# Kernel optimization log

Hardware: AMD Instinct MI355X
Metric: run time of the kernel (lower is better)

The kernel has to match this reference:

```python
import jax, jax.numpy as jnp
import numpy as np

B, P, ENC = 128, 625, 512
A, E, H, V = 256, 256, 512, 70
START_TOK, END_TOK = 68, 69


def setup_inputs() -> dict:
    key = jax.random.key(0)
    ks = jax.random.split(key, 20)
    w = lambda k, shape: jax.random.normal(k, shape, jnp.float32) * 0.02
    return {
        "encoder_out": jax.random.normal(ks[0], (B, P, ENC), jnp.float32),
        "emb": w(ks[1], (V, E)),
        "We": w(ks[2], (ENC, A)), "be": jnp.zeros((A,), jnp.float32),
        "Wd": w(ks[3], (H, A)),   "bd": jnp.zeros((A,), jnp.float32),
        "wf": w(ks[4], (A,)),     "bf": jnp.zeros((), jnp.float32),
        "Wh0": w(ks[5], (ENC, H)), "bh0": jnp.zeros((H,), jnp.float32),
        "Wc0": w(ks[6], (ENC, H)), "bc0": jnp.zeros((H,), jnp.float32),
        "Wb": w(ks[7], (H, ENC)), "bb": jnp.zeros((ENC,), jnp.float32),
        "Wih": w(ks[8], (E + ENC, 4 * H)), "Whh": w(ks[9], (H, 4 * H)),
        "bih": jnp.zeros((4 * H,), jnp.float32), "bhh": jnp.zeros((4 * H,), jnp.float32),
        "Wfc": w(ks[10], (H, V)), "bfc": jnp.zeros((V,), jnp.float32),
        "decode_lengths": 70,
    }


def _decode(encoder_out, emb, We, be, Wd, bd, wf, bf, Wh0, bh0, Wc0, bc0,
            Wb, bb, Wih, Whh, bih, bhh, Wfc, bfc, decode_lengths):
    enc = encoder_out  # [B, P, ENC]
    batch = enc.shape[0]
    # encoder_att projection is constant across timesteps -> hoist out of loop
    att1 = enc @ We + be                      # [B, P, A]
    mean_enc = enc.mean(axis=1)               # [B, ENC]
    h0 = mean_enc @ Wh0 + bh0                 # [B, H]
    c0 = mean_enc @ Wc0 + bc0                 # [B, H]
    emb0 = emb[jnp.full((batch,), START_TOK)]  # [B, E]
    lstm_b = bih + bhh

    def step(carry, _):
        h, c, emb_t, done = carry
        att2 = h @ Wd + bd                                            # [B, A]
        e = jnp.einsum('bpa,a->bp', jax.nn.relu(att1 + att2[:, None, :]), wf) + bf
        alpha = jax.nn.softmax(e, axis=1)                             # [B, P]
        awe = jnp.einsum('bp,bpe->be', alpha, enc)                    # [B, ENC]
        awe = jax.nn.sigmoid(h @ Wb + bb) * awe                       # gated
        gates = jnp.concatenate([emb_t, awe], axis=1) @ Wih + h @ Whh + lstm_b
        i_, f_, g_, o_ = jnp.split(gates, 4, axis=1)                  # torch order i,f,g,o
        c_new = jax.nn.sigmoid(f_) * c + jax.nn.sigmoid(i_) * jnp.tanh(g_)
        h_new = jax.nn.sigmoid(o_) * jnp.tanh(c_new)
        preds = h_new @ Wfc + bfc                                     # [B, V] (dropout eval = id)
        preds_out = jnp.where(done, 0.0, preds)                       # zeros after early break
        done_new = done | (jnp.argmax(preds) == END_TOK)              # flat argmax, as in torch
        emb_new = emb[jnp.argmax(preds, axis=-1)]                     # greedy feedback
        return (h_new, c_new, emb_new, done_new), preds_out

    init = (h0, c0, emb0, jnp.array(False))
    _, preds_seq = jax.lax.scan(step, init, None, length=decode_lengths)
    return jnp.transpose(preds_seq, (1, 0, 2))  # [B, T, V]


def reference(encoder_out, emb, We, be, Wd, bd, wf, bf, Wh0, bh0, Wc0, bc0,
              Wb, bb, Wih, Whh, bih, bhh, Wfc, bfc, decode_lengths):
    return _decode(encoder_out, emb, We, be, Wd, bd, wf, bf, Wh0, bh0, Wc0, bc0,
                   Wb, bb, Wih, Whh, bih, bhh, Wfc, bfc, decode_lengths)
```

## Files before the change

kernel.cpp:

```cpp
#include <hip/hip_runtime.h>
#include <math.h>

#define Bn 128
#define Pn 625
#define ENCn 512
#define An 256
#define En 256
#define Hn 512
#define Vn 70
#define G4n 2048
#define STARTT 68
#define ENDT 69
#define NCHUNK 5
#define PCH 125
#define PSTRIDE 520
#define KSPLIT 16
#define KCH 80


__global__ __launch_bounds__(256) void k_mean(const float* __restrict__ enc,
                                              float* __restrict__ mean_enc) {
  int b = blockIdx.x, t = threadIdx.x;
  const float* e = enc + (size_t)b * Pn * ENCn;
  float s0 = 0.f, s1 = 0.f;
  for (int p = 0; p < Pn; ++p) {
    s0 += e[(size_t)p * ENCn + t];
    s1 += e[(size_t)p * ENCn + t + 256];
  }
  mean_enc[b * ENCn + t] = s0 * (1.0f / 625.0f);
  mean_enc[b * ENCn + t + 256] = s1 * (1.0f / 625.0f);
}

__global__ __launch_bounds__(512) void k_init(const float* __restrict__ mean_enc,
                       const float* __restrict__ Wh0, const float* __restrict__ bh0,
                       const float* __restrict__ Wc0, const float* __restrict__ bc0,
                       const float* __restrict__ emb,
                       float* __restrict__ h0, float* __restrict__ c0,
                       float* __restrict__ emb_t, int* __restrict__ done_arr) {
  int b = blockIdx.x, t = threadIdx.x;
  const float* W = blockIdx.y ? Wc0 : Wh0;
  const float* bias = blockIdx.y ? bc0 : bh0;
  float* out = blockIdx.y ? c0 : h0;
  __shared__ float ms[ENCn];
  ms[t] = mean_enc[b * ENCn + t];
  __syncthreads();
  float s = bias[t];
  for (int k = 0; k < ENCn; ++k) s += ms[k] * W[k * Hn + t];
  out[b * Hn + t] = s;
  if (blockIdx.y == 0 && t < En) emb_t[b * En + t] = emb[STARTT * En + t];
  if (blockIdx.y == 0 && b == 0 && t == 0) done_arr[0] = 0;
}

__global__ __launch_bounds__(256) void k_att1(const float* __restrict__ Am,
                       const float* __restrict__ We,
                       const float* __restrict__ be, float* __restrict__ att1) {
  __shared__ float sA[16][128];
  __shared__ float sB[16][128];
  int n0 = blockIdx.x * 128, m0 = blockIdx.y * 128;
  int t = threadIdx.x;
  int tm = (t >> 4) * 8, tn = (t & 15) * 8;
  float acc[8][8];
#pragma unroll
  for (int i = 0; i < 8; ++i)
#pragma unroll
    for (int j = 0; j < 8; ++j) acc[i][j] = 0.f;
  for (int k0 = 0; k0 < 512; k0 += 16) {
    __syncthreads();
#pragma unroll
    for (int i = 0; i < 8; ++i) {
      int idx = t + i * 256;
      int mm = idx >> 4, kk = idx & 15;
      sA[kk][mm] = Am[(size_t)(m0 + mm) * 512 + k0 + kk];
      int kk2 = idx >> 7, nn = idx & 127;
      sB[kk2][nn] = We[(size_t)(k0 + kk2) * 256 + n0 + nn];
    }
    __syncthreads();
#pragma unroll
    for (int kk = 0; kk < 16; ++kk) {
      float a[8], bq[8];
      *(float4*)&a[0] = *(const float4*)&sA[kk][tm];
      *(float4*)&a[4] = *(const float4*)&sA[kk][tm + 4];
      *(float4*)&bq[0] = *(const float4*)&sB[kk][tn];
      *(float4*)&bq[4] = *(const float4*)&sB[kk][tn + 4];
#pragma unroll
      for (int i = 0; i < 8; ++i)
#pragma unroll
        for (int j = 0; j < 8; ++j) acc[i][j] += a[i] * bq[j];
    }
  }
  float ber[8];
  *(float4*)&ber[0] = *(const float4*)&be[n0 + tn];
  *(float4*)&ber[4] = *(const float4*)&be[n0 + tn + 4];
#pragma unroll
  for (int i = 0; i < 8; ++i) {
    float o[8];
#pragma unroll
    for (int j = 0; j < 8; ++j) o[j] = acc[i][j] + ber[j];
    *(float4*)&att1[(size_t)(m0 + tm + i) * An + n0 + tn] = *(float4*)&o[0];
    *(float4*)&att1[(size_t)(m0 + tm + i) * An + n0 + tn + 4] = *(float4*)&o[4];
  }
}


__global__ __launch_bounds__(256) void k_proj(const float* __restrict__ h,
                       const float* __restrict__ Wd, const float* __restrict__ bd,
                       const float* __restrict__ Wb, const float* __restrict__ bbv,
                       float* __restrict__ att2, float* __restrict__ gate,
                       const float* __restrict__ preds,
                       const int* __restrict__ done_prev, int* __restrict__ done_cur,
                       int do_flat) {
  int t = threadIdx.x;
  if (blockIdx.x == Bn) {
    if (!do_flat) return;
    __shared__ float sv[256];
    __shared__ int si[256];
    float bv = -1e30f; int bi = 0x7fffffff;
    for (int i = t; i < Bn * Vn; i += 256) {
      float v = preds[i];
      if (v > bv) { bv = v; bi = i; }
    }
    sv[t] = bv; si[t] = bi;
    __syncthreads();
    for (int s = 128; s > 0; s >>= 1) {
      if (t < s) {
        if (sv[t + s] > sv[t] || (sv[t + s] == sv[t] && si[t + s] < si[t])) {
          sv[t] = sv[t + s]; si[t] = si[t + s];
        }
      }
      __syncthreads();
    }
    if (t == 0) *done_cur = (*done_prev) | (si[0] == ENDT ? 1 : 0);
    return;
  }
  int b = blockIdx.x;
  __shared__ float hsh[Hn];
  hsh[t] = h[b * Hn + t];
  hsh[t + 256] = h[b * Hn + t + 256];
  __syncthreads();
  float s0 = bd[t];
  float s1 = bbv[t], s2 = bbv[t + 256];
  for (int k = 0; k < Hn; ++k) {
    float hv = hsh[k];
    s0 += hv * Wd[(size_t)k * An + t];
    s1 += hv * Wb[(size_t)k * ENCn + t];
    s2 += hv * Wb[(size_t)k * ENCn + t + 256];
  }
  att2[b * An + t] = s0;
  gate[b * ENCn + t] = 1.f / (1.f + expf(-s1));
  gate[b * ENCn + t + 256] = 1.f / (1.f + expf(-s2));
}

__global__ __launch_bounds__(256) void k_attn(const float* __restrict__ att1,
                       const float* __restrict__ att2,
                       const float* __restrict__ wf, const float* __restrict__ bfp,
                       const float* __restrict__ enc, float* __restrict__ part) {
  int c = blockIdx.x, b = blockIdx.y, t = threadIdx.x;
  int lane = t & 63, wv = t >> 6;
  int p0 = c * PCH;
  __shared__ float es[PCH];
  __shared__ float red[256];
  float4 a2 = ((const float4*)(att2 + b * An))[lane];
  float4 wfr = ((const float4*)wf)[lane];
  float bfv = *bfp;
  const float* a1b = att1 + ((size_t)b * Pn + p0) * An;
  for (int p = wv; p < PCH; p += 4) {
    float4 v = ((const float4*)(a1b + (size_t)p * An))[lane];
    float s = fmaxf(v.x + a2.x, 0.f) * wfr.x
            + fmaxf(v.y + a2.y, 0.f) * wfr.y
            + fmaxf(v.z + a2.z, 0.f) * wfr.z
            + fmaxf(v.w + a2.w, 0.f) * wfr.w;
    for (int o = 32; o > 0; o >>= 1) s += __shfl_down(s, o, 64);
    if (lane == 0) es[p] = s + bfv;
  }
  __syncthreads();
  float m = -1e30f;
  for (int i = t; i < PCH; i += 256) m = fmaxf(m, es[i]);
  red[t] = m;
  __syncthreads();
  for (int s = 128; s > 0; s >>= 1) {
    if (t < s) red[t] = fmaxf(red[t], red[t + s]);
    __syncthreads();
  }
  m = red[0];
  __syncthreads();
  float lp = 0.f;
  for (int i = t; i < PCH; i += 256) {
    float e2 = expf(es[i] - m);
    es[i] = e2;
    lp += e2;
  }
  red[t] = lp;
  __syncthreads();
  for (int s = 128; s > 0; s >>= 1) {
    if (t < s) red[t] += red[t + s];
    __syncthreads();
  }
  float l = red[0];
  float acc0 = 0.f, acc1 = 0.f;
  const float* ebase = enc + ((size_t)b * Pn + p0) * ENCn;
  for (int p = 0; p < PCH; ++p) {
    float wp = es[p];
    acc0 += wp * ebase[(size_t)p * ENCn + t];
    acc1 += wp * ebase[(size_t)p * ENCn + t + 256];
  }
  float* pp = part + (size_t)(b * NCHUNK + c) * PSTRIDE;
  if (t == 0) { pp[0] = m; pp[1] = l; }
  pp[8 + t] = acc0;
  pp[8 + t + 256] = acc1;
}

__global__ __launch_bounds__(256) void k_combine(const float* __restrict__ part,
                       const float* __restrict__ gate, float* __restrict__ awe) {
  int b = blockIdx.x, t = threadIdx.x;
  const float* pb = part + (size_t)b * NCHUNK * PSTRIDE;
  float M = -1e30f;
#pragma unroll
  for (int c = 0; c < NCHUNK; ++c) M = fmaxf(M, pb[c * PSTRIDE]);
  float L = 0.f, sc[NCHUNK];
#pragma unroll
  for (int c = 0; c < NCHUNK; ++c) {
    float s = expf(pb[c * PSTRIDE] - M);
    sc[c] = s;
    L += s * pb[c * PSTRIDE + 1];
  }
  float inv = 1.f / L;
  float a0 = 0.f, a1 = 0.f;
#pragma unroll
  for (int c = 0; c < NCHUNK; ++c) {
    a0 += sc[c] * pb[c * PSTRIDE + 8 + t];
    a1 += sc[c] * pb[c * PSTRIDE + 8 + t + 256];
  }
  awe[b * ENCn + t] = a0 * inv * gate[b * ENCn + t];
  awe[b * ENCn + t + 256] = a1 * inv * gate[b * ENCn + t + 256];
}

__global__ __launch_bounds__(256) void k_gates(const float* __restrict__ embt,
                       const float* __restrict__ awe, const float* __restrict__ h,
                       const float* __restrict__ Wih, const float* __restrict__ Whh,
                       float* __restrict__ gp) {
  int n0 = blockIdx.x * 64;
  int sI = blockIdx.y;
  int k0 = sI * KCH;
  int t = threadIdx.x;
  int tc = t & 15, tg = t >> 4;
  int nc = n0 + tc * 4;
  float4 acc[8];
#pragma unroll
  for (int r = 0; r < 8; ++r) acc[r] = make_float4(0.f, 0.f, 0.f, 0.f);
  for (int kk = 0; kk < KCH; kk += 4) {
    int k = k0 + kk;
    const float* wbase = (k < 768) ? (Wih + (size_t)k * G4n + nc)
                                   : (Whh + (size_t)(k - 768) * G4n + nc);
    float4 w0 = *(const float4*)(wbase);
    float4 w1 = *(const float4*)(wbase + G4n);
    float4 w2 = *(const float4*)(wbase + 2 * G4n);
    float4 w3 = *(const float4*)(wbase + 3 * G4n);
#pragma unroll
    for (int r = 0; r < 8; ++r) {
      int row = tg * 8 + r;
      float4 xv;
      if (k < 256)      xv = *(const float4*)(embt + row * En + k);
      else if (k < 768) xv = *(const float4*)(awe + row * ENCn + (k - 256));
      else              xv = *(const float4*)(h + row * Hn + (k - 768));
      acc[r].x += xv.x * w0.x + xv.y * w1.x + xv.z * w2.x + xv.w * w3.x;
      acc[r].y += xv.x * w0.y + xv.y * w1.y + xv.z * w2.y + xv.w * w3.y;
      acc[r].z += xv.x * w0.z + xv.y * w1.z + xv.z * w2.z + xv.w * w3.z;
      acc[r].w += xv.x * w0.w + xv.y * w1.w + xv.z * w2.w + xv.w * w3.w;
    }
  }
#pragma unroll
  for (int r = 0; r < 8; ++r)
    *(float4*)(gp + ((size_t)sI * Bn + tg * 8 + r) * G4n + nc) = acc[r];
}

__global__ __launch_bounds__(512) void k_lstm(const float* __restrict__ gp,
                       const float* __restrict__ bih, const float* __restrict__ bhh,
                       const float* __restrict__ c_in, float* __restrict__ c_out,
                       float* __restrict__ h_out,
                       const float* __restrict__ Wfc, const float* __restrict__ bfc,
                       const float* __restrict__ emb, float* __restrict__ preds,
                       float* __restrict__ emb_next, float* __restrict__ out,
                       const int* __restrict__ done_t, int step, int T) {
  int b = blockIdx.x, t = threadIdx.x;
  float gi = bih[t] + bhh[t];
  float gf = bih[t + 512] + bhh[t + 512];
  float gg = bih[t + 1024] + bhh[t + 1024];
  float go = bih[t + 1536] + bhh[t + 1536];
  for (int s = 0; s < KSPLIT; ++s) {
    const float* row = gp + ((size_t)s * Bn + b) * G4n;
    gi += row[t];
    gf += row[t + 512];
    gg += row[t + 1024];
    go += row[t + 1536];
  }
  float cv = (1.f / (1.f + expf(-gf))) * c_in[b * Hn + t]
           + (1.f / (1.f + expf(-gi))) * tanhf(gg);
  float hv = (1.f / (1.f + expf(-go))) * tanhf(cv);
  c_out[b * Hn + t] = cv;
  h_out[b * Hn + t] = hv;
  __shared__ float hs[Hn];
  __shared__ float ps[Vn];
  __shared__ int tokS;
  hs[t] = hv;
  __syncthreads();
  int lane = t & 63, wvi = t >> 6;
  for (int v = wvi; v < Vn; v += 8) {
    float s = 0.f;
    for (int k = lane; k < Hn; k += 64) s += hs[k] * Wfc[(size_t)k * Vn + v];
    for (int o = 32; o > 0; o >>= 1) s += __shfl_down(s, o, 64);
    if (lane == 0) ps[v] = s + bfc[v];
  }
  __syncthreads();
  int done = *done_t;
  if (t < Vn) {
    float pv = ps[t];
    preds[b * Vn + t] = pv;
    out[((size_t)b * T + step) * Vn + t] = done ? 0.f : pv;
  }
  if (t == 0) {
    float bv = ps[0]; int bi = 0;
    for (int v = 1; v < Vn; ++v)
      if (ps[v] > bv) { bv = ps[v]; bi = v; }
    tokS = bi;
  }
  __syncthreads();
  if (t < En) emb_next[b * En + t] = emb[tokS * En + t];
}


extern "C" void kernel_launch(void* const* d_in, const int* in_sizes, int n_in,
                              void* d_out, int out_size, void* d_ws, size_t ws_size,
                              hipStream_t stream) {
  const float* enc = (const float*)d_in[0];
  const float* emb = (const float*)d_in[1];
  const float* We  = (const float*)d_in[2];
  const float* be  = (const float*)d_in[3];
  const float* Wd  = (const float*)d_in[4];
  const float* bd  = (const float*)d_in[5];
  const float* wf  = (const float*)d_in[6];
  const float* bf  = (const float*)d_in[7];
  const float* Wh0 = (const float*)d_in[8];
  const float* bh0 = (const float*)d_in[9];
  const float* Wc0 = (const float*)d_in[10];
  const float* bc0 = (const float*)d_in[11];
  const float* Wb  = (const float*)d_in[12];
  const float* bb  = (const float*)d_in[13];
  const float* Wih = (const float*)d_in[14];
  const float* Whh = (const float*)d_in[15];
  const float* bih = (const float*)d_in[16];
  const float* bhh = (const float*)d_in[17];
  const float* Wfc = (const float*)d_in[18];
  const float* bfc = (const float*)d_in[19];
  int T = out_size / (Bn * Vn);

  float* w = (float*)d_ws;
  size_t off = 0;
  float* att1 = w + off;     off += (size_t)Bn * Pn * An;
  float* mean_enc = w + off; off += Bn * ENCn;
  float* hb0 = w + off;      off += Bn * Hn;
  float* hb1 = w + off;      off += Bn * Hn;
  float* cb0 = w + off;      off += Bn * Hn;
  float* cb1 = w + off;      off += Bn * Hn;
  float* eb0 = w + off;      off += Bn * En;
  float* eb1 = w + off;      off += Bn * En;
  float* att2 = w + off;     off += Bn * An;
  float* gate = w + off;     off += Bn * ENCn;
  float* part = w + off;     off += (size_t)Bn * NCHUNK * PSTRIDE;
  float* awe = w + off;      off += Bn * ENCn;
  float* gatesP = w + off;   off += (size_t)KSPLIT * Bn * G4n;
  float* preds = w + off;    off += Bn * Vn;
  off = (off + 255) & ~(size_t)255;
  int* done_arr = (int*)(w + off);

  float* hbuf[2] = {hb0, hb1};
  float* cbuf[2] = {cb0, cb1};
  float* ebuf[2] = {eb0, eb1};

  k_mean<<<Bn, 256, 0, stream>>>(enc, mean_enc);
  k_init<<<dim3(Bn, 2), 512, 0, stream>>>(mean_enc, Wh0, bh0, Wc0, bc0, emb,
                                          hb0, cb0, eb0, done_arr);
  k_att1<<<dim3(2, 625), 256, 0, stream>>>(enc, We, be, att1);

  int cur = 0;
  for (int t = 0; t < T; ++t) {
    int nxt = cur ^ 1;
    k_proj<<<Bn + 1, 256, 0, stream>>>(hbuf[cur], Wd, bd, Wb, bb, att2, gate, preds,
                                       done_arr + (t > 0 ? t - 1 : 0), done_arr + t,
                                       t > 0 ? 1 : 0);
    k_attn<<<dim3(NCHUNK, Bn), 256, 0, stream>>>(att1, att2, wf, bf, enc, part);
    k_combine<<<Bn, 256, 0, stream>>>(part, gate, awe);
    k_gates<<<dim3(32, KSPLIT), 256, 0, stream>>>(ebuf[cur], awe, hbuf[cur], Wih, Whh, gatesP);
    k_lstm<<<Bn, 512, 0, stream>>>(gatesP, bih, bhh, cbuf[cur], cbuf[nxt], hbuf[nxt],
                                   Wfc, bfc, emb, preds, ebuf[nxt], (float*)d_out,
                                   done_arr + t, t, T);
    cur = nxt;
  }
}
```

Baseline: 10.13 ms.

## Restructure decode step: fold projection into LSTM kernel and split attention score/value

The per-step pipeline drops from five launches to four. The h@Wd / h@Wb projection moves into extra blocks of the LSTM kernel, which recompute h_new for pairs of rows. Attention is split into a scores kernel and a value kernel that rescales each chunk by the global softmax stats. The chunk partials are summed inside the gates GEMM instead of in a separate combine kernel. The flat argmax now reduces 128 per-row maxima instead of scanning all predictions. This removes launches and serialized small kernels, at the cost of redundant LSTM recomputation and five-way partial reads repeated across the gate blocks.

```diff
diff --git a/kernel.cpp b/kernel.cpp
--- a/kernel.cpp
+++ b/kernel.cpp
@@ -13,9 +13,32 @@
 #define ENDT 69
 #define NCHUNK 5
 #define PCH 125
-#define PSTRIDE 520
+#define SSTRIDE 640
+#define PAWS (Bn * 512)
 #define KSPLIT 16
 #define KCH 80
+
+__device__ __forceinline__ float sigm(float x) { return 1.f / (1.f + expf(-x)); }
+
+__device__ __forceinline__ float lstm_h(const float* __restrict__ gp, int b, int u,
+                                        const float* __restrict__ bih,
+                                        const float* __restrict__ bhh,
+                                        float c_in, float* cv_out) {
+  float gi = bih[u] + bhh[u];
+  float gf = bih[u + 512] + bhh[u + 512];
+  float gg = bih[u + 1024] + bhh[u + 1024];
+  float go = bih[u + 1536] + bhh[u + 1536];
+  for (int s = 0; s < KSPLIT; ++s) {
+    const float* row = gp + ((size_t)s * Bn + b) * G4n;
+    gi += row[u];
+    gf += row[u + 512];
+    gg += row[u + 1024];
+    go += row[u + 1536];
+  }
+  float cv = sigm(gf) * c_in + sigm(gi) * tanhf(gg);
+  *cv_out = cv;
+  return sigm(go) * tanhf(cv);
+}
 
 
 __global__ __launch_bounds__(256) void k_mean(const float* __restrict__ enc,
@@ -101,38 +124,11 @@
   }
 }
 
-
-__global__ __launch_bounds__(256) void k_proj(const float* __restrict__ h,
+__global__ __launch_bounds__(256) void k_proj0(const float* __restrict__ h,
                        const float* __restrict__ Wd, const float* __restrict__ bd,
                        const float* __restrict__ Wb, const float* __restrict__ bbv,
-                       float* __restrict__ att2, float* __restrict__ gate,
-                       const float* __restrict__ preds,
-                       const int* __restrict__ done_prev, int* __restrict__ done_cur,
-                       int do_flat) {
-  int t = threadIdx.x;
-  if (blockIdx.x == Bn) {
-    if (!do_flat) return;
-    __shared__ float sv[256];
-    __shared__ int si[256];
-    float bv = -1e30f; int bi = 0x7fffffff;
-    for (int i = t; i < Bn * Vn; i += 256) {
-      float v = preds[i];
-      if (v > bv) { bv = v; bi = i; }
-    }
-    sv[t] = bv; si[t] = bi;
-    __syncthreads();
-    for (int s = 128; s > 0; s >>= 1) {
-      if (t < s) {
-        if (sv[t + s] > sv[t] || (sv[t + s] == sv[t] && si[t + s] < si[t])) {
-          sv[t] = sv[t + s]; si[t] = si[t + s];
-        }
-      }
-      __syncthreads();
-    }
-    if (t == 0) *done_cur = (*done_prev) | (si[0] == ENDT ? 1 : 0);
-    return;
-  }
-  int b = blockIdx.x;
+                       float* __restrict__ att2, float* __restrict__ gate) {
+  int b = blockIdx.x, t = threadIdx.x;
   __shared__ float hsh[Hn];
   hsh[t] = h[b * Hn + t];
   hsh[t + 256] = h[b * Hn + t + 256];
@@ -146,15 +142,36 @@
     s2 += hv * Wb[(size_t)k * ENCn + t + 256];
   }
   att2[b * An + t] = s0;
-  gate[b * ENCn + t] = 1.f / (1.f + expf(-s1));
-  gate[b * ENCn + t + 256] = 1.f / (1.f + expf(-s2));
-}
-
-__global__ __launch_bounds__(256) void k_attn(const float* __restrict__ att1,
+  gate[b * ENCn + t] = sigm(s1);
+  gate[b * ENCn + t + 256] = sigm(s2);
+}
+
+
+__global__ __launch_bounds__(256) void k_score(const float* __restrict__ att1,
                        const float* __restrict__ att2,
                        const float* __restrict__ wf, const float* __restrict__ bfp,
-                       const float* __restrict__ enc, float* __restrict__ part) {
-  int c = blockIdx.x, b = blockIdx.y, t = threadIdx.x;
+                       float* __restrict__ scores, float* __restrict__ stats,
+                       const float* __restrict__ rowval, const int* __restrict__ rowidx,
+                       int* __restrict__ done_f, int do_flat) {
+  int t = threadIdx.x;
+  if (blockIdx.x == 640) {
+    if (!do_flat) return;
+    __shared__ float sv[128];
+    __shared__ int si[128];
+    if (t < 128) { sv[t] = rowval[t]; si[t] = t * Vn + rowidx[t]; }
+    __syncthreads();
+    for (int s = 64; s > 0; s >>= 1) {
+      if (t < s) {
+        if (sv[t + s] > sv[t] || (sv[t + s] == sv[t] && si[t + s] < si[t])) {
+          sv[t] = sv[t + s]; si[t] = si[t + s];
+        }
+      }
+      __syncthreads();
+    }
+    if (t == 0 && si[0] == ENDT) *done_f = 1;
+    return;
+  }
+  int c = blockIdx.x % NCHUNK, b = blockIdx.x / NCHUNK;
   int lane = t & 63, wv = t >> 6;
   int p0 = c * PCH;
   __shared__ float es[PCH];
@@ -195,47 +212,47 @@
     if (t < s) red[t] += red[t + s];
     __syncthreads();
   }
-  float l = red[0];
-  float acc0 = 0.f, acc1 = 0.f;
-  const float* ebase = enc + ((size_t)b * Pn + p0) * ENCn;
+  if (t < PCH) scores[b * SSTRIDE + p0 + t] = es[t];
+  if (t == 0) {
+    stats[(b * NCHUNK + c) * 2] = m;
+    stats[(b * NCHUNK + c) * 2 + 1] = red[0];
+  }
+}
+
+__global__ __launch_bounds__(256) void k_value(const float* __restrict__ scores,
+                       const float* __restrict__ stats,
+                       const float* __restrict__ gate,
+                       const float* __restrict__ enc, float* __restrict__ paw) {
+  int c = blockIdx.x % NCHUNK, b = blockIdx.x / NCHUNK, t = threadIdx.x;
+  int p0 = c * PCH;
+  float mv[NCHUNK], lv[NCHUNK];
+  float M = -1e30f;
+#pragma unroll
+  for (int cc = 0; cc < NCHUNK; ++cc) {
+    mv[cc] = stats[(b * NCHUNK + cc) * 2];
+    lv[cc] = stats[(b * NCHUNK + cc) * 2 + 1];
+    M = fmaxf(M, mv[cc]);
+  }
+  float L = 0.f;
+#pragma unroll
+  for (int cc = 0; cc < NCHUNK; ++cc) L += expf(mv[cc] - M) * lv[cc];
+  float scinv = expf(mv[c] - M) * (1.f / L);
+  float2 g = ((const float2*)(gate + b * ENCn))[t];
+  const float* sp = scores + b * SSTRIDE + p0;
+  const float2* eb2 = (const float2*)(enc + ((size_t)b * Pn + p0) * ENCn);
+  float a0 = 0.f, a1 = 0.f;
+#pragma unroll 5
   for (int p = 0; p < PCH; ++p) {
-    float wp = es[p];
-    acc0 += wp * ebase[(size_t)p * ENCn + t];
-    acc1 += wp * ebase[(size_t)p * ENCn + t + 256];
-  }
-  float* pp = part + (size_t)(b * NCHUNK + c) * PSTRIDE;
-  if (t == 0) { pp[0] = m; pp[1] = l; }
-  pp[8 + t] = acc0;
-  pp[8 + t + 256] = acc1;
-}
-
-__global__ __launch_bounds__(256) void k_combine(const float* __restrict__ part,
-                       const float* __restrict__ gate, float* __restrict__ awe) {
-  int b = blockIdx.x, t = threadIdx.x;
-  const float* pb = part + (size_t)b * NCHUNK * PSTRIDE;
-  float M = -1e30f;
-#pragma unroll
-  for (int c = 0; c < NCHUNK; ++c) M = fmaxf(M, pb[c * PSTRIDE]);
-  float L = 0.f, sc[NCHUNK];
-#pragma unroll
-  for (int c = 0; c < NCHUNK; ++c) {
-    float s = expf(pb[c * PSTRIDE] - M);
-    sc[c] = s;
-    L += s * pb[c * PSTRIDE + 1];
-  }
-  float inv = 1.f / L;
-  float a0 = 0.f, a1 = 0.f;
-#pragma unroll
-  for (int c = 0; c < NCHUNK; ++c) {
-    a0 += sc[c] * pb[c * PSTRIDE + 8 + t];
-    a1 += sc[c] * pb[c * PSTRIDE + 8 + t + 256];
-  }
-  awe[b * ENCn + t] = a0 * inv * gate[b * ENCn + t];
-  awe[b * ENCn + t + 256] = a1 * inv * gate[b * ENCn + t + 256];
+    float wp = sp[p] * scinv;
+    float2 v = eb2[(size_t)p * 256 + t];
+    a0 += wp * v.x;
+    a1 += wp * v.y;
+  }
+  ((float2*)(paw + (size_t)(c * Bn + b) * 512))[t] = make_float2(a0 * g.x, a1 * g.y);
 }
 
 __global__ __launch_bounds__(256) void k_gates(const float* __restrict__ embt,
-                       const float* __restrict__ awe, const float* __restrict__ h,
+                       const float* __restrict__ paw, const float* __restrict__ h,
                        const float* __restrict__ Wih, const float* __restrict__ Whh,
                        float* __restrict__ gp) {
   int n0 = blockIdx.x * 64;
@@ -259,9 +276,22 @@
     for (int r = 0; r < 8; ++r) {
       int row = tg * 8 + r;
       float4 xv;
-      if (k < 256)      xv = *(const float4*)(embt + row * En + k);
-      else if (k < 768) xv = *(const float4*)(awe + row * ENCn + (k - 256));
-      else              xv = *(const float4*)(h + row * Hn + (k - 768));
+      if (k < 256) {
+        xv = *(const float4*)(embt + row * En + k);
+      } else if (k < 768) {
+        const float* pb = paw + (size_t)row * 512 + (k - 256);
+        float4 x0 = *(const float4*)(pb);
+        float4 x1 = *(const float4*)(pb + PAWS);
+        float4 x2 = *(const float4*)(pb + 2 * PAWS);
+        float4 x3 = *(const float4*)(pb + 3 * PAWS);
+        float4 x4 = *(const float4*)(pb + 4 * PAWS);
+        xv.x = (((x0.x + x1.x) + x2.x) + x3.x) + x4.x;
+        xv.y = (((x0.y + x1.y) + x2.y) + x3.y) + x4.y;
+        xv.z = (((x0.z + x1.z) + x2.z) + x3.z) + x4.z;
+        xv.w = (((x0.w + x1.w) + x2.w) + x3.w) + x4.w;
+      } else {
+        xv = *(const float4*)(h + row * Hn + (k - 768));
+      }
       acc[r].x += xv.x * w0.x + xv.y * w1.x + xv.z * w2.x + xv.w * w3.x;
       acc[r].y += xv.x * w0.y + xv.y * w1.y + xv.z * w2.y + xv.w * w3.y;
       acc[r].z += xv.x * w0.z + xv.y * w1.z + xv.z * w2.z + xv.w * w3.z;
@@ -278,53 +308,74 @@
                        const float* __restrict__ c_in, float* __restrict__ c_out,
                        float* __restrict__ h_out,
                        const float* __restrict__ Wfc, const float* __restrict__ bfc,
-                       const float* __restrict__ emb, float* __restrict__ preds,
+                       const float* __restrict__ emb,
+                       float* __restrict__ rowval, int* __restrict__ rowidx,
                        float* __restrict__ emb_next, float* __restrict__ out,
-                       const int* __restrict__ done_t, int step, int T) {
-  int b = blockIdx.x, t = threadIdx.x;
-  float gi = bih[t] + bhh[t];
-  float gf = bih[t + 512] + bhh[t + 512];
-  float gg = bih[t + 1024] + bhh[t + 1024];
-  float go = bih[t + 1536] + bhh[t + 1536];
-  for (int s = 0; s < KSPLIT; ++s) {
-    const float* row = gp + ((size_t)s * Bn + b) * G4n;
-    gi += row[t];
-    gf += row[t + 512];
-    gg += row[t + 1024];
-    go += row[t + 1536];
-  }
-  float cv = (1.f / (1.f + expf(-gf))) * c_in[b * Hn + t]
-           + (1.f / (1.f + expf(-gi))) * tanhf(gg);
-  float hv = (1.f / (1.f + expf(-go))) * tanhf(cv);
-  c_out[b * Hn + t] = cv;
-  h_out[b * Hn + t] = hv;
-  __shared__ float hs[Hn];
+                       const int* __restrict__ done_t, int step, int T,
+                       const float* __restrict__ Wd, const float* __restrict__ bd,
+                       const float* __restrict__ Wb, const float* __restrict__ bbv,
+                       float* __restrict__ att2, float* __restrict__ gate,
+                       int do_proj) {
+  int blk = blockIdx.x, t = threadIdx.x;
+  __shared__ float hs[1024];
   __shared__ float ps[Vn];
   __shared__ int tokS;
-  hs[t] = hv;
-  __syncthreads();
-  int lane = t & 63, wvi = t >> 6;
-  for (int v = wvi; v < Vn; v += 8) {
-    float s = 0.f;
-    for (int k = lane; k < Hn; k += 64) s += hs[k] * Wfc[(size_t)k * Vn + v];
-    for (int o = 32; o > 0; o >>= 1) s += __shfl_down(s, o, 64);
-    if (lane == 0) ps[v] = s + bfc[v];
-  }
-  __syncthreads();
-  int done = *done_t;
-  if (t < Vn) {
-    float pv = ps[t];
-    preds[b * Vn + t] = pv;
-    out[((size_t)b * T + step) * Vn + t] = done ? 0.f : pv;
-  }
-  if (t == 0) {
-    float bv = ps[0]; int bi = 0;
-    for (int v = 1; v < Vn; ++v)
-      if (ps[v] > bv) { bv = ps[v]; bi = v; }
-    tokS = bi;
-  }
-  __syncthreads();
-  if (t < En) emb_next[b * En + t] = emb[tokS * En + t];
+  if (blk < Bn) {
+    int b = blk;
+    float cv;
+    float hv = lstm_h(gp, b, t, bih, bhh, c_in[b * Hn + t], &cv);
+    c_out[b * Hn + t] = cv;
+    h_out[b * Hn + t] = hv;
+    hs[t] = hv;
+    __syncthreads();
+    int lane = t & 63, wvi = t >> 6;
+    for (int v = wvi; v < Vn; v += 8) {
+      float s = 0.f;
+      for (int k = lane; k < Hn; k += 64) s += hs[k] * Wfc[(size_t)k * Vn + v];
+      for (int o = 32; o > 0; o >>= 1) s += __shfl_down(s, o, 64);
+      if (lane == 0) ps[v] = s + bfc[v];
+    }
+    __syncthreads();
+    int done = *done_t;
+    if (t < Vn) out[((size_t)b * T + step) * Vn + t] = done ? 0.f : ps[t];
+    if (t == 0) {
+      float bv = ps[0]; int bi = 0;
+      for (int v = 1; v < Vn; ++v)
+        if (ps[v] > bv) { bv = ps[v]; bi = v; }
+      rowval[b] = bv; rowidx[b] = bi; tokS = bi;
+    }
+    __syncthreads();
+    if (t < En) emb_next[b * En + t] = emb[tokS * En + t];
+  } else {
+    if (!do_proj) return;
+    int r0 = (blk - Bn) * 2;
+#pragma unroll
+    for (int rr = 0; rr < 2; ++rr) {
+      int b = r0 + rr;
+      float cv;
+      hs[rr * 512 + t] = lstm_h(gp, b, t, bih, bhh, c_in[b * Hn + t], &cv);
+    }
+    __syncthreads();
+#pragma unroll
+    for (int i = 0; i < 3; ++i) {
+      int idx = i * 512 + t;
+      int row = idx / 768, col = idx % 768;
+      int b = r0 + row;
+      const float* hrow = hs + row * 512;
+      if (col < 256) {
+        float s = bd[col];
+#pragma unroll 4
+        for (int k = 0; k < Hn; ++k) s += hrow[k] * Wd[(size_t)k * An + col];
+        att2[b * An + col] = s;
+      } else {
+        int cc = col - 256;
+        float s = bbv[cc];
+#pragma unroll 4
+        for (int k = 0; k < Hn; ++k) s += hrow[k] * Wb[(size_t)k * ENCn + cc];
+        gate[b * ENCn + cc] = sigm(s);
+      }
+    }
+  }
 }
 
 
@@ -365,11 +416,13 @@
   float* eb1 = w + off;      off += Bn * En;
   float* att2 = w + off;     off += Bn * An;
   float* gate = w + off;     off += Bn * ENCn;
-  float* part = w + off;     off += (size_t)Bn * NCHUNK * PSTRIDE;
-  float* awe = w + off;      off += Bn * ENCn;
+  float* scores = w + off;   off += (size_t)Bn * SSTRIDE;
+  float* stats = w + off;    off += Bn * NCHUNK * 2;
+  float* paw = w + off;      off += (size_t)NCHUNK * Bn * 512;
   float* gatesP = w + off;   off += (size_t)KSPLIT * Bn * G4n;
-  float* preds = w + off;    off += Bn * Vn;
+  float* rowval = w + off;   off += 256;
   off = (off + 255) & ~(size_t)255;
+  int* rowidx = (int*)(w + off); off += 256;
   int* done_arr = (int*)(w + off);
 
   float* hbuf[2] = {hb0, hb1};
@@ -380,19 +433,19 @@
   k_init<<<dim3(Bn, 2), 512, 0, stream>>>(mean_enc, Wh0, bh0, Wc0, bc0, emb,
                                           hb0, cb0, eb0, done_arr);
   k_att1<<<dim3(2, 625), 256, 0, stream>>>(enc, We, be, att1);
+  k_proj0<<<Bn, 256, 0, stream>>>(hb0, Wd, bd, Wb, bb, att2, gate);
 
   int cur = 0;
   for (int t = 0; t < T; ++t) {
     int nxt = cur ^ 1;
-    k_proj<<<Bn + 1, 256, 0, stream>>>(hbuf[cur], Wd, bd, Wb, bb, att2, gate, preds,
-                                       done_arr + (t > 0 ? t - 1 : 0), done_arr + t,
-                                       t > 0 ? 1 : 0);
-    k_attn<<<dim3(NCHUNK, Bn), 256, 0, stream>>>(att1, att2, wf, bf, enc, part);
-    k_combine<<<Bn, 256, 0, stream>>>(part, gate, awe);
-    k_gates<<<dim3(32, KSPLIT), 256, 0, stream>>>(ebuf[cur], awe, hbuf[cur], Wih, Whh, gatesP);
-    k_lstm<<<Bn, 512, 0, stream>>>(gatesP, bih, bhh, cbuf[cur], cbuf[nxt], hbuf[nxt],
-                                   Wfc, bfc, emb, preds, ebuf[nxt], (float*)d_out,
-                                   done_arr + t, t, T);
+    k_score<<<641, 256, 0, stream>>>(att1, att2, wf, bf, scores, stats,
+                                     rowval, rowidx, done_arr, t > 0 ? 1 : 0);
+    k_value<<<640, 256, 0, stream>>>(scores, stats, gate, enc, paw);
+    k_gates<<<dim3(32, KSPLIT), 256, 0, stream>>>(ebuf[cur], paw, hbuf[cur], Wih, Whh, gatesP);
+    k_lstm<<<192, 512, 0, stream>>>(gatesP, bih, bhh, cbuf[cur], cbuf[nxt], hbuf[nxt],
+                                    Wfc, bfc, emb, rowval, rowidx, ebuf[nxt], (float*)d_out,
+                                    done_arr, t, T,
+                                    Wd, bd, Wb, bb, att2, gate, t < T - 1 ? 1 : 0);
     cur = nxt;
   }
 }
```

After: 15.77 ms. +55.7%, slower.
